# Performance work log

Hardware: AMD Instinct MI355X
Metric: run time of the kernel (lower is better)

Reference implementation:

```python
import jax, jax.numpy as jnp
import numpy as np
from jax.scipy.linalg import block_diag

N_STATE, N_INPUT, HORIZON = 32, 16, 64


def setup_inputs() -> dict:
    key = jax.random.key(0)
    kA, kB, kC, kx = jax.random.split(key, 4)
    n_all = N_STATE + N_INPUT
    A = jax.random.normal(kA, (N_STATE, N_STATE), dtype=jnp.float32)
    B = jax.random.normal(kB, (N_STATE, N_INPUT), dtype=jnp.float32)
    Craw = jax.random.normal(kC, (HORIZON, n_all, n_all), dtype=jnp.float32)
    # symmetric positive-definite stage costs -> nonsingular KKT system
    C = jnp.einsum('tij,tkj->tik', Craw, Craw) / jnp.sqrt(jnp.float32(n_all)) \
        + jnp.eye(n_all, dtype=jnp.float32)
    x0 = jax.random.normal(kx, (N_STATE,), dtype=jnp.float32)
    return {"A": A, "B": B, "C": C, "T": HORIZON, "x0": x0}


def reference(A, B, C, T, x0):
    n_state = A.shape[0]
    n_input = B.shape[1]
    n_all = n_state + n_input
    dt = A.dtype

    # cost_mat: block-diagonal [n_all*T, n_all*T]
    cost_mat = block_diag(*C)

    # dynamics: [n_state*T, n_all*T]
    AB = jnp.concatenate((A, B), axis=1)              # [n_state, n_all]
    AB_blk = block_diag(*([AB] * (T - 1)))            # [(T-1)*n_state, (T-1)*n_all]
    dynamics = jnp.zeros((n_state * T, n_all * T), dtype=dt)
    dynamics = dynamics.at[:n_state, :n_state].set(jnp.eye(n_state, dtype=dt))
    dynamics = dynamics.at[n_state:n_state + (T - 1) * n_state,
                           :(T - 1) * n_all].set(AB_blk)
    # -I coupling entries: row n_state*t + i, col n_all*t + i, t=1..T-1
    t = jnp.arange(1, T)
    rows = (n_state * t)[:, None] + jnp.arange(n_state)[None, :]
    cols = (n_all * t)[:, None] + jnp.arange(n_state)[None, :]
    dynamics = dynamics.at[rows, cols].set(jnp.asarray(-1.0, dt))

    zero_mat = jnp.zeros((n_state * T, n_state * T), dtype=dt)
    full_mat = jnp.block([[cost_mat, dynamics.T],
                          [dynamics, zero_mat]])      # [(n_all+n_state)*T]^2

    # rhs: zeros except x0 at the start of the dynamics block
    sol = jnp.zeros(n_all * T + n_state * T, dtype=dt)
    sol = sol.at[n_all * T: n_all * T + n_state].set(x0)

    tau_mu = jnp.linalg.solve(full_mat, sol[:, None])[:, 0]
    tau_star = tau_mu[:n_all * T]
    mu_star = tau_mu[n_all * T:]
    return tau_star, mu_star
```

## Files before the change

kernel.cpp:

```cpp
#include <hip/hip_runtime.h>


namespace {

constexpr int NS  = 32;
constexpr int NI  = 16;
constexpr int NA  = 48;
constexpr int TT  = 64;
constexpr int NTH = 256;
constexpr int NBLK = 64;

using ull = unsigned long long;

__device__ __forceinline__ void fma4(float4& a, float s, const float4& b) {
  a.x += s * b.x; a.y += s * b.y; a.z += s * b.z; a.w += s * b.w;
}
__device__ __forceinline__ void fms4(float4& a, float s, const float4& b) {
  a.x -= s * b.x; a.y -= s * b.y; a.z -= s * b.z; a.w -= s * b.w;
}
__device__ __forceinline__ float dot4(const float4& a, const float4& b) {
  return a.x * b.x + a.y * b.y + a.z * b.z + a.w * b.w;
}
__device__ __forceinline__ float rdlane(float v, int l) {
  return __int_as_float(__builtin_amdgcn_readlane(__float_as_int(v), l));
}

__device__ __forceinline__ ull ald(const ull* p) {
  return __hip_atomic_load(p, __ATOMIC_RELAXED, __HIP_MEMORY_SCOPE_AGENT);
}
__device__ __forceinline__ void ast(ull* p, ull v) {
  __hip_atomic_store(p, v, __ATOMIC_RELAXED, __HIP_MEMORY_SCOPE_AGENT);
}
__device__ __forceinline__ ull pack2(float x, float y) {
  return (ull)__float_as_uint(x) | ((ull)__float_as_uint(y) << 32);
}
__device__ __forceinline__ float2 unpack2(ull v) {
  return make_float2(__uint_as_float((unsigned)v),
                     __uint_as_float((unsigned)(v >> 32)));
}
__device__ __forceinline__ float4 ald4(const ull* p) {
  ull lo = ald(p), hi = ald(p + 1);
  float2 a = unpack2(lo), b = unpack2(hi);
  return make_float4(a.x, a.y, b.x, b.y);
}
__device__ __forceinline__ void ast4(ull* p, const float4& v) {
  ast(p, pack2(v.x, v.y)); ast(p + 1, pack2(v.z, v.w));
}

__device__ __forceinline__ unsigned fld(const unsigned* f) {
  return __hip_atomic_load(f, __ATOMIC_RELAXED, __HIP_MEMORY_SCOPE_AGENT);
}
__device__ __forceinline__ void fst(unsigned* f) {
  __hip_atomic_store(f, 1u, __ATOMIC_RELAXED, __HIP_MEMORY_SCOPE_AGENT);
}
__device__ __forceinline__ void waitf(const unsigned* f) {
  if (threadIdx.x == 0)
    while (fld(f) == 0) __builtin_amdgcn_s_sleep(1);
  __syncthreads();
}
__device__ __forceinline__ void setf(unsigned* f) {
  asm volatile("s_waitcnt vmcnt(0)" ::: "memory");
  __syncthreads();
  if (threadIdx.x == 0) fst(f);
}

template<int K>
__device__ __forceinline__ void tile_outer(const float* Acol0, int lda,
                                           const float* Bcol0, int ldb,
                                           float4 acc[4]) {
  #pragma unroll
  for (int m = 0; m < K; ++m) {
    const float4 va = *(const float4*)(Acol0 + m * lda);
    const float4 vb = *(const float4*)(Bcol0 + m * ldb);
    fma4(acc[0], va.x, vb); fma4(acc[1], va.y, vb);
    fma4(acc[2], va.z, vb); fma4(acc[3], va.w, vb);
  }
}

template<int KQ>
__device__ __forceinline__ void tile_dot(const float* Arow0, int lda,
                                         const float* Brow0, int ldb,
                                         float acc[4][4]) {
  #pragma unroll
  for (int q = 0; q < KQ; ++q) {
    float4 va[4], vb[4];
    #pragma unroll
    for (int r = 0; r < 4; ++r) va[r] = *(const float4*)(Arow0 + r * lda + 4 * q);
    #pragma unroll
    for (int c = 0; c < 4; ++c) vb[c] = *(const float4*)(Brow0 + c * ldb + 4 * q);
    #pragma unroll
    for (int r = 0; r < 4; ++r)
      #pragma unroll
      for (int c = 0; c < 4; ++c) acc[r][c] += dot4(va[r], vb[c]);
  }
}

__device__ __forceinline__ float step_dot(const float4 m[8], float x) {
  float a0 = 0.f, a1 = 0.f, a2 = 0.f, a3 = 0.f;
  #pragma unroll
  for (int q = 0; q < 8; ++q) {
    a0 += rdlane(x, 4 * q + 0) * m[q].x;
    a1 += rdlane(x, 4 * q + 1) * m[q].y;
    a2 += rdlane(x, 4 * q + 2) * m[q].z;
    a3 += rdlane(x, 4 * q + 3) * m[q].w;
  }
  return (a0 + a1) + (a2 + a3);
}

__device__ __forceinline__ int nlev(int rm) {
  return (rm == TT - 1) ? 0 : (32 - __clz(TT - 1 - rm));
}

__global__ __launch_bounds__(NTH, 1) void lqr_all(
    const float* __restrict__ A, const float* __restrict__ Bm,
    const float* __restrict__ C, const float* __restrict__ x0,
    float* __restrict__ out,
    float* __restrict__ Sb0, float* __restrict__ Sb1,
    float* __restrict__ Mall, unsigned* __restrict__ flg) {
  __shared__ float sC [NA][NA];
  __shared__ float sAB[NS][NA];
  __shared__ float sRiST[NS][NI];
  __shared__ float sBRi [NS][NI];
  __shared__ float sAi[NS][NS], sCi[NS][NS], sJi[NS][NS];
  __shared__ float sAj[NS][NS], sCj[NS][NS], sJj[NS][NS];
  __shared__ float sAjT[NS][36];
  __shared__ float sV[NS][NS], sU[NS][NS];
  __shared__ float sY1[NS][NS], sY2[NS][NS], sW[NS][NS];
  __shared__ float sX[NS][NS], sZm[NS][NS];
  __shared__ float sG[NS][NA], sFu[NI][NA], sK[NI][NS], sK2[NI][NS];
  __shared__ float sXt0[NS], sXt1[NS];

  const int t = ((blockIdx.x & 7) << 3) | (blockIdx.x >> 3);
  const int tid = threadIdx.x, lane = tid & 63, wid = tid >> 6;
  unsigned* wr = flg;
  unsigned* rd = flg + 448;
  unsigned* mf = flg + 832;

  {
    const float* Ct = C + (size_t)t * NA * NA;
    for (int e = tid; e < NA * NA; e += NTH) sC[e / NA][e % NA] = Ct[e];
    for (int e = tid; e < NS * NA; e += NTH) {
      int i = e / NA, j = e % NA;
      sAB[i][j] = (j < NS) ? A[i * NS + j] : Bm[i * NI + (j - NS)];
    }
    __syncthreads();
    if (wid < 2 && lane < 48) {
      const int c = lane;
      float f[NI];
      if (c < NI) {
        #pragma unroll
        for (int i = 0; i < NI; ++i) f[i] = sC[NS + i][NS + c];
      } else {
        const int a = c - NI;
        if (wid == 0) {
          #pragma unroll
          for (int i = 0; i < NI; ++i) f[i] = sC[a][NS + i];
        } else {
          #pragma unroll
          for (int i = 0; i < NI; ++i) f[i] = sAB[a][NS + i];
        }
      }
      #pragma unroll
      for (int k = 0; k < NI; ++k) {
        float mi[NI];
        #pragma unroll
        for (int i = 0; i < NI; ++i) mi[i] = rdlane(f[i], k);
        const float inv = 1.0f / mi[k];
        f[k] *= inv;
        #pragma unroll
        for (int i = 0; i < NI; ++i) if (i != k) f[i] -= mi[i] * f[k];
      }
      if (c >= NI) {
        const int a = c - NI;
        float* D = (wid == 0) ? &sRiST[a][0] : &sBRi[a][0];
        #pragma unroll
        for (int i = 0; i < NI; ++i) D[i] = f[i];
      }
    }
    __syncthreads();
    ull* outA = (ull*)(Sb0 + (size_t)t * 3072);
    ull* outC = outA + 512;
    ull* outJ = outA + 1024;
    if (tid < 64) {
      const int a = tid >> 3, b = tid & 7;
      float acc[4][4];
      #pragma unroll
      for (int r = 0; r < 4; ++r)
        #pragma unroll
        for (int c = 0; c < 4; ++c) acc[r][c] = 0.f;
      tile_dot<4>(&sRiST[4 * a][0], NI, &sC[4 * b][NS], NA, acc);
      #pragma unroll
      for (int r = 0; r < 4; ++r) {
        const float4 q4 = *(const float4*)&sC[4 * a + r][4 * b];
        const float4 v = make_float4(q4.x - acc[r][0], q4.y - acc[r][1],
                                     q4.z - acc[r][2], q4.w - acc[r][3]);
        *(float4*)&sJi[4 * a + r][4 * b] = v;
        ast4(outJ + ((4 * a + r) * NS + 4 * b) / 2, v);
      }
    } else if (tid < 128) {
      const int q = tid - 64, a = q >> 3, b = q & 7;
      float acc[4][4];
      #pragma unroll
      for (int r = 0; r < 4; ++r)
        #pragma unroll
        for (int c = 0; c < 4; ++c) acc[r][c] = 0.f;
      tile_dot<4>(&sBRi[4 * a][0], NI, &sC[4 * b][NS], NA, acc);
      #pragma unroll
      for (int r = 0; r < 4; ++r) {
        const float4 a4 = *(const float4*)&sAB[4 * a + r][4 * b];
        const float4 v = make_float4(a4.x - acc[r][0], a4.y - acc[r][1],
                                     a4.z - acc[r][2], a4.w - acc[r][3]);
        *(float4*)&sAi[4 * a + r][4 * b] = v;
        ast4(outA + ((4 * a + r) * NS + 4 * b) / 2, v);
      }
    } else if (tid < 192) {
      const int q = tid - 128, a = q >> 3, b = q & 7;
      float acc[4][4];
      #pragma unroll
      for (int r = 0; r < 4; ++r)
        #pragma unroll
        for (int c = 0; c < 4; ++c) acc[r][c] = 0.f;
      tile_dot<4>(&sBRi[4 * a][0], NI, &sAB[4 * b][NS], NA, acc);
      #pragma unroll
      for (int r = 0; r < 4; ++r) {
        const float4 v = make_float4(acc[r][0], acc[r][1], acc[r][2], acc[r][3]);
        *(float4*)&sCi[4 * a + r][4 * b] = v;
        ast4(outC + ((4 * a + r) * NS + 4 * b) / 2, v);
      }
    }
  }
  setf(&wr[0 * 64 + t]);

  auto combine = [&]() {
    #pragma unroll
    for (int r = 0; r < 4; ++r) {
      const int e = tid + 256 * r, i = e >> 5, j = e & 31;
      sAjT[j][i] = sAj[i][j];
    }
    if (tid < 64) {
      const int a = tid >> 3, b = tid & 7;
      float4 acc[4] = {make_float4(0,0,0,0), make_float4(0,0,0,0),
                       make_float4(0,0,0,0), make_float4(0,0,0,0)};
      tile_outer<NS>(&sCi[0][4 * a], NS, &sJj[0][4 * b], NS, acc);
      if (a == b) { acc[0].x += 1.f; acc[1].y += 1.f; acc[2].z += 1.f; acc[3].w += 1.f; }
      #pragma unroll
      for (int r = 0; r < 4; ++r) *(float4*)&sX[4 * a + r][4 * b] = acc[r];
    }
    __syncthreads();
    if (wid < 2) {
      const int c = lane;
      float f[NS];
      if (c < NS) {
        #pragma unroll
        for (int i = 0; i < NS; ++i) f[i] = sX[i][c];
      } else if (wid == 0) {
        #pragma unroll
        for (int i = 0; i < NS; ++i) f[i] = sAi[i][c - NS];
      } else {
        #pragma unroll
        for (int i = 0; i < NS; ++i) f[i] = sCi[i][c - NS];
      }
      #pragma unroll
      for (int k = 0; k < NS; ++k) {
        float mi[NS];
        #pragma unroll
        for (int i = 0; i < NS; ++i) mi[i] = rdlane(f[i], k);
        const float inv = 1.0f / mi[k];
        f[k] *= inv;
        #pragma unroll
        for (int i = 0; i < NS; ++i) if (i != k) f[i] -= mi[i] * f[k];
      }
      if (c >= NS) {
        const int col = c - NS;
        if (wid == 0) {
          #pragma unroll
          for (int i = 0; i < NS; ++i) sV[i][col] = f[i];
        } else {
          #pragma unroll
          for (int i = 0; i < NS; ++i) sU[i][col] = f[i];
        }
      }
    }
    __syncthreads();
    if (tid < 192) {
      const int grp = tid >> 6, q = tid & 63, a = q >> 3, b = q & 7;
      float4 acc[4] = {make_float4(0,0,0,0), make_float4(0,0,0,0),
                       make_float4(0,0,0,0), make_float4(0,0,0,0)};
      if (grp == 0) {
        tile_outer<NS>(&sJj[0][4 * a], NS, &sV[0][4 * b], NS, acc);
        #pragma unroll
        for (int r = 0; r < 4; ++r) *(float4*)&sW[4 * a + r][4 * b] = acc[r];
      } else if (grp == 1) {
        tile_outer<NS>(&sAjT[0][4 * a], 36, &sV[0][4 * b], NS, acc);
        #pragma unroll
        for (int r = 0; r < 4; ++r) *(float4*)&sX[4 * a + r][4 * b] = acc[r];
      } else {
        tile_outer<NS>(&sAjT[0][4 * a], 36, &sU[0][4 * b], NS, acc);
        #pragma unroll
        for (int r = 0; r < 4; ++r) *(float4*)&sZm[4 * a + r][4 * b] = acc[r];
      }
    }
    __syncthreads();
    if (tid < 64) {
      const int a = tid >> 3, b = tid & 7;
      float4 acc[4] = {make_float4(0,0,0,0), make_float4(0,0,0,0),
                       make_float4(0,0,0,0), make_float4(0,0,0,0)};
      tile_outer<NS>(&sAi[0][4 * a], NS, &sW[0][4 * b], NS, acc);
      #pragma unroll
      for (int r = 0; r < 4; ++r) {
        const float4 j4 = *(const float4*)&sJi[4 * a + r][4 * b];
        acc[r].x += j4.x; acc[r].y += j4.y; acc[r].z += j4.z; acc[r].w += j4.w;
        *(float4*)&sY1[4 * a + r][4 * b] = acc[r];
      }
    } else if (tid < 128) {
      const int q = tid - 64, a = q >> 3, b = q & 7;
      float acc[4][4];
      #pragma unroll
      for (int r = 0; r < 4; ++r)
        #pragma unroll
        for (int c = 0; c < 4; ++c) acc[r][c] = 0.f;
      tile_dot<8>(&sZm[4 * a][0], NS, &sAj[4 * b][0], NS, acc);
      #pragma unroll
      for (int r = 0; r < 4; ++r) {
        const float4 c4 = *(const float4*)&sCj[4 * a + r][4 * b];
        *(float4*)&sY2[4 * a + r][4 * b] =
            make_float4(acc[r][0] + c4.x, acc[r][1] + c4.y,
                        acc[r][2] + c4.z, acc[r][3] + c4.w);
      }
    }
    __syncthreads();
    ((ull*)sAi)[tid] = ((const ull*)sX)[tid];
    ((ull*)sAi)[tid + 256] = ((const ull*)sX)[tid + 256];
    ((ull*)sCi)[tid] = ((const ull*)sY2)[tid];
    ((ull*)sCi)[tid + 256] = ((const ull*)sY2)[tid + 256];
    ((ull*)sJi)[tid] = ((const ull*)sY1)[tid];
    ((ull*)sJi)[tid + 256] = ((const ull*)sY1)[tid + 256];
    __syncthreads();
  };

  for (int l = 0; l < 6; ++l) {
    const int off = 1 << l;
    const int rm = t + off;
    if (rm < TT) {
      const int nlv = nlev(rm);
      const int v = (l < nlv) ? l : nlv;
      const float* Sin = (v & 1) ? Sb1 : Sb0;
      float* Sout = ((l + 1) & 1) ? Sb1 : Sb0;
      ull* Eo = (ull*)(Sout + (size_t)t * 3072);
      waitf(&wr[v * 64 + rm]);
      const ull* Ej = (const ull*)(Sin + (size_t)rm * 3072);
      {
        ull r0 = ald(Ej + tid),        r1 = ald(Ej + 256 + tid);
        ull r2 = ald(Ej + 512 + tid),  r3 = ald(Ej + 768 + tid);
        ull r4 = ald(Ej + 1024 + tid), r5 = ald(Ej + 1280 + tid);
        ((ull*)sAj)[tid] = r0; ((ull*)sAj)[tid + 256] = r1;
        ((ull*)sCj)[tid] = r2; ((ull*)sCj)[tid + 256] = r3;
        ((ull*)sJj)[tid] = r4; ((ull*)sJj)[tid + 256] = r5;
      }
      __syncthreads();
      if (v == l && tid == 0) fst(&rd[l * 64 + rm]);
      combine();
      if (l >= 1 && t >= (off >> 1)) waitf(&rd[(l - 1) * 64 + t]);
      ast(Eo + tid,        ((const ull*)sAi)[tid]);
      ast(Eo + 256 + tid,  ((const ull*)sAi)[tid + 256]);
      ast(Eo + 512 + tid,  ((const ull*)sCi)[tid]);
      ast(Eo + 768 + tid,  ((const ull*)sCi)[tid + 256]);
      ast(Eo + 1024 + tid, ((const ull*)sJi)[tid]);
      ast(Eo + 1280 + tid, ((const ull*)sJi)[tid + 256]);
      setf(&wr[(l + 1) * 64 + t]);
    }
  }

  auto kmat = [&](int tau, bool hasP, float (*Pm)[NS], float (*Kd)[NS], bool wM) {
    const int ui = tid / 12, uk = tid - 12 * ui;
    float4 cr0 = make_float4(0,0,0,0), cr1 = make_float4(0,0,0,0);
    float4 cr2 = make_float4(0,0,0,0), cr3 = make_float4(0,0,0,0);
    if (tid < 48) {
      const float* Ct = C + (size_t)tau * NA * NA;
      cr0 = *(const float4*)&Ct[(NS + 4 * ui + 0) * NA + 4 * uk];
      cr1 = *(const float4*)&Ct[(NS + 4 * ui + 1) * NA + 4 * uk];
      cr2 = *(const float4*)&Ct[(NS + 4 * ui + 2) * NA + 4 * uk];
      cr3 = *(const float4*)&Ct[(NS + 4 * ui + 3) * NA + 4 * uk];
    }
    if (hasP) {
      if (tid < 96) {
        const int gi = tid / 12, gk = tid - 12 * gi;
        float4 acc[4] = {make_float4(0,0,0,0), make_float4(0,0,0,0),
                         make_float4(0,0,0,0), make_float4(0,0,0,0)};
        tile_outer<NS>(&Pm[0][4 * gi], NS, &sAB[0][4 * gk], NA, acc);
        #pragma unroll
        for (int r = 0; r < 4; ++r) *(float4*)&sG[4 * gi + r][4 * gk] = acc[r];
      }
    } else {
      for (int e = tid; e < NS * NA; e += NTH) sG[e / NA][e % NA] = 0.f;
    }
    __syncthreads();
    if (tid < 48) {
      float4 acc[4] = {cr0, cr1, cr2, cr3};
      tile_outer<NS>(&sAB[0][NS + 4 * ui], NA, &sG[0][4 * uk], NA, acc);
      #pragma unroll
      for (int r = 0; r < 4; ++r) *(float4*)&sFu[4 * ui + r][4 * uk] = acc[r];
    }
    __syncthreads();
    if (wid == 0) {
      const int col = (lane < 16) ? (NS + lane) : (lane - 16);
      float f[NI];
      #pragma unroll
      for (int i = 0; i < NI; ++i) f[i] = sFu[i][col];
      #pragma unroll
      for (int k = 0; k < NI; ++k) {
        float mi[NI];
        #pragma unroll
        for (int i = 0; i < NI; ++i) mi[i] = rdlane(f[i], k);
        const float inv = 1.0f / mi[k];
        f[k] *= inv;
        #pragma unroll
        for (int i = 0; i < NI; ++i) if (i != k) f[i] -= mi[i] * f[k];
      }
      if (lane >= 16 && lane < 48) {
        const int b = lane - 16;
        #pragma unroll
        for (int i = 0; i < NI; ++i) Kd[i][b] = f[i];
      }
    }
    __syncthreads();
    if (wM && tid < 64) {
      const int ma = tid >> 3, mb = tid & 7;
      float4 a0 = *(const float4*)&sAB[4 * ma + 0][4 * mb];
      float4 a1 = *(const float4*)&sAB[4 * ma + 1][4 * mb];
      float4 a2 = *(const float4*)&sAB[4 * ma + 2][4 * mb];
      float4 a3 = *(const float4*)&sAB[4 * ma + 3][4 * mb];
      #pragma unroll
      for (int q = 0; q < 4; ++q) {
        const float4 vf0 = *(const float4*)&sAB[4 * ma + 0][NS + 4 * q];
        const float4 vf1 = *(const float4*)&sAB[4 * ma + 1][NS + 4 * q];
        const float4 vf2 = *(const float4*)&sAB[4 * ma + 2][NS + 4 * q];
        const float4 vf3 = *(const float4*)&sAB[4 * ma + 3][NS + 4 * q];
        #pragma unroll
        for (int d = 0; d < 4; ++d) {
          const float4 vkk = *(const float4*)&Kd[4 * q + d][4 * mb];
          const float s0 = (d == 0) ? vf0.x : (d == 1) ? vf0.y : (d == 2) ? vf0.z : vf0.w;
          const float s1 = (d == 0) ? vf1.x : (d == 1) ? vf1.y : (d == 2) ? vf1.z : vf1.w;
          const float s2 = (d == 0) ? vf2.x : (d == 1) ? vf2.y : (d == 2) ? vf2.z : vf2.w;
          const float s3 = (d == 0) ? vf3.x : (d == 1) ? vf3.y : (d == 2) ? vf3.z : vf3.w;
          fms4(a0, s0, vkk); fms4(a1, s1, vkk); fms4(a2, s2, vkk); fms4(a3, s3, vkk);
        }
      }
      ull* Mt = (ull*)(Mall + (size_t)tau * NS * NS);
      ast4(Mt + (4 * ma + 0) * 16 + 2 * mb, a0);
      ast4(Mt + (4 * ma + 1) * 16 + 2 * mb, a1);
      ast4(Mt + (4 * ma + 2) * 16 + 2 * mb, a2);
      ast4(Mt + (4 * ma + 3) * 16 + 2 * mb, a3);
    }
    __syncthreads();
  };

  if (t >= 1) kmat(t - 1, true, sJi, sK, true);
  if (t == TT - 1) kmat(TT - 1, false, nullptr, sK2, false);
  setf(&mf[t]);

  {
    if (tid < NBLK) {
      while (fld(&mf[tid]) == 0) __builtin_amdgcn_s_sleep(1);
    }
    __syncthreads();
    if (wid == 0) {
      const int i = lane;
      if (i < NS) {
        const ull* Mg = (const ull*)Mall;
        float4 mA[8], mB[8];
        float x = x0[i];
        if (t == 1) sXt1[i] = x;
        if (t >= 1) {
          #pragma unroll
          for (int q = 0; q < 8; ++q) mA[q] = ald4(Mg + 0 * 512 + i * 16 + 2 * q);
        }
        if (t >= 2) {
          #pragma unroll
          for (int q = 0; q < 8; ++q) mB[q] = ald4(Mg + 1 * 512 + i * 16 + 2 * q);
        }
        for (int s = 0; s < t; s += 2) {
          x = step_dot(mA, x);
          if (s + 1 == t - 1) sXt1[i] = x;
          if (s + 2 < t) {
            #pragma unroll
            for (int q = 0; q < 8; ++q)
              mA[q] = ald4(Mg + (s + 2) * 512 + i * 16 + 2 * q);
          }
          if (s + 1 < t) {
            x = step_dot(mB, x);
            if (s + 2 == t - 1) sXt1[i] = x;
            if (s + 3 < t) {
              #pragma unroll
              for (int q = 0; q < 8; ++q)
                mB[q] = ald4(Mg + (s + 3) * 512 + i * 16 + 2 * q);
            }
          }
        }
        sXt0[i] = x;
        out[t * NA + i] = x;
      }
    }
    __syncthreads();
  }

  {
    if (t >= 1 && tid < NI) {
      const float4* Kr = (const float4*)&sK[tid][0];
      const float4* xr = (const float4*)sXt1;
      float acc = 0.f;
      #pragma unroll
      for (int q = 0; q < 8; ++q) acc += dot4(Kr[q], xr[q]);
      out[(t - 1) * NA + NS + tid] = -acc;
    } else if (tid >= NI && tid < NI + NS) {
      const int i = tid - NI;
      const float4* Pr = (const float4*)&sJi[i][0];
      const float4* xr = (const float4*)sXt0;
      float acc = 0.f;
      #pragma unroll
      for (int q = 0; q < 8; ++q) acc += dot4(Pr[q], xr[q]);
      out[NA * TT + t * NS + i] = (t == 0) ? -acc : acc;
    } else if (t == TT - 1 && tid >= 192 && tid < 192 + NI) {
      const int i = tid - 192;
      const float4* Kr = (const float4*)&sK2[i][0];
      const float4* xr = (const float4*)sXt0;
      float acc = 0.f;
      #pragma unroll
      for (int q = 0; q < 8; ++q) acc += dot4(Kr[q], xr[q]);
      out[(TT - 1) * NA + NS + i] = -acc;
    }
  }
}

}

extern "C" void kernel_launch(void* const* d_in, const int* in_sizes, int n_in,
                              void* d_out, int out_size, void* d_ws, size_t ws_size,
                              hipStream_t stream) {
  const float* A  = (const float*)d_in[0];
  const float* Bm = (const float*)d_in[1];
  const float* C  = (const float*)d_in[2];
  const float* x0 = (const float*)d_in[4];
  float* out = (float*)d_out;

  float* Sb0 = (float*)d_ws;
  float* Sb1 = Sb0 + (size_t)TT * 3072;
  float* Mall = Sb1 + (size_t)TT * 3072;
  unsigned* flg = (unsigned*)(Mall + (size_t)TT * NS * NS);

  hipMemsetAsync(flg, 0, 4096, stream);
  hipLaunchKernelGGL(lqr_all, dim3(NBLK), dim3(NTH), 0, stream,
                     A, Bm, C, x0, out, Sb0, Sb1, Mall, flg);
}
```

Baseline: 126.6 us.

## Switch parallel scan to radix-4 levels with dual concurrent combines

Replaces the six-level radix-2 associative scan over time steps with a three-level radix-4 scan. Each block now waits for and loads up to three neighbour elements per level. Two of the combines run concurrently on half-block partitions, followed by a full-block combine. This cuts the number of cross-block synchronisation rounds and global flag waits, in exchange for more work per level, counted read-done flags, and heavier shared-memory use. Shared buffers are aliased to fit the extra staging.

New measurement: 139.6 us. 1.1x slower.

```diff
diff --git a/kernel.cpp b/kernel.cpp
--- a/kernel.cpp
+++ b/kernel.cpp
@@ -107,8 +107,8 @@
   return (a0 + a1) + (a2 + a3);
 }
 
-__device__ __forceinline__ int nlev(int rm) {
-  return (rm == TT - 1) ? 0 : (32 - __clz(TT - 1 - rm));
+__device__ __forceinline__ int nlev4(int rm) {
+  return (rm < 48) ? 3 : (rm < 60) ? 2 : (rm < 63) ? 1 : 0;
 }
 
 __global__ __launch_bounds__(NTH, 1) void lqr_all(
@@ -117,24 +117,25 @@
     float* __restrict__ out,
     float* __restrict__ Sb0, float* __restrict__ Sb1,
     float* __restrict__ Mall, unsigned* __restrict__ flg) {
-  __shared__ float sC [NA][NA];
+  __shared__ float sScr[NA * NA];
   __shared__ float sAB[NS][NA];
   __shared__ float sRiST[NS][NI];
   __shared__ float sBRi [NS][NI];
   __shared__ float sAi[NS][NS], sCi[NS][NS], sJi[NS][NS];
-  __shared__ float sAj[NS][NS], sCj[NS][NS], sJj[NS][NS];
-  __shared__ float sAjT[NS][36];
-  __shared__ float sV[NS][NS], sU[NS][NS];
-  __shared__ float sY1[NS][NS], sY2[NS][NS], sW[NS][NS];
-  __shared__ float sX[NS][NS], sZm[NS][NS];
-  __shared__ float sG[NS][NA], sFu[NI][NA], sK[NI][NS], sK2[NI][NS];
+  __shared__ float sE[3][3][NS][NS];
+  __shared__ float sAjT[2][NS][36];
+  __shared__ float sXs[2][NS][NS], sVs[2][NS][NS], sUs[2][NS][NS];
+  __shared__ float sWs[2][NS][NS], sZs[2][NS][NS];
+  __shared__ float sK[NI][NS], sK2[NI][NS];
   __shared__ float sXt0[NS], sXt1[NS];
 
   const int t = ((blockIdx.x & 7) << 3) | (blockIdx.x >> 3);
   const int tid = threadIdx.x, lane = tid & 63, wid = tid >> 6;
-  unsigned* wr = flg;
-  unsigned* rd = flg + 448;
-  unsigned* mf = flg + 832;
+  unsigned* wr  = flg;
+  unsigned* rdc = flg + 256;
+  unsigned* mf  = flg + 448;
+
+  float (*sC)[NA] = (float(*)[NA])sScr;
 
   {
     const float* Ct = C + (size_t)t * NA * NA;
@@ -231,20 +232,23 @@
   }
   setf(&wr[0 * 64 + t]);
 
-  auto combine = [&]() {
+  auto combine_full = [&](float (*RA)[NS], float (*RC)[NS], float (*RJ)[NS]) {
+    float (*T)[36] = sAjT[0];
+    float (*X)[NS] = sXs[0]; float (*V)[NS] = sVs[0]; float (*U)[NS] = sUs[0];
+    float (*W)[NS] = sWs[0]; float (*Z)[NS] = sZs[0];
     #pragma unroll
     for (int r = 0; r < 4; ++r) {
       const int e = tid + 256 * r, i = e >> 5, j = e & 31;
-      sAjT[j][i] = sAj[i][j];
+      T[j][i] = RA[i][j];
     }
     if (tid < 64) {
       const int a = tid >> 3, b = tid & 7;
       float4 acc[4] = {make_float4(0,0,0,0), make_float4(0,0,0,0),
                        make_float4(0,0,0,0), make_float4(0,0,0,0)};
-      tile_outer<NS>(&sCi[0][4 * a], NS, &sJj[0][4 * b], NS, acc);
+      tile_outer<NS>(&sCi[0][4 * a], NS, &RJ[0][4 * b], NS, acc);
       if (a == b) { acc[0].x += 1.f; acc[1].y += 1.f; acc[2].z += 1.f; acc[3].w += 1.f; }
       #pragma unroll
-      for (int r = 0; r < 4; ++r) *(float4*)&sX[4 * a + r][4 * b] = acc[r];
+      for (int r = 0; r < 4; ++r) *(float4*)&X[4 * a + r][4 * b] = acc[r];
     }
     __syncthreads();
     if (wid < 2) {
@@ -252,7 +256,7 @@
       float f[NS];
       if (c < NS) {
         #pragma unroll
-        for (int i = 0; i < NS; ++i) f[i] = sX[i][c];
+        for (int i = 0; i < NS; ++i) f[i] = X[i][c];
       } else if (wid == 0) {
         #pragma unroll
         for (int i = 0; i < NS; ++i) f[i] = sAi[i][c - NS];
@@ -272,13 +276,9 @@
       }
       if (c >= NS) {
         const int col = c - NS;
-        if (wid == 0) {
-          #pragma unroll
-          for (int i = 0; i < NS; ++i) sV[i][col] = f[i];
-        } else {
-          #pragma unroll
-          for (int i = 0; i < NS; ++i) sU[i][col] = f[i];
-        }
+        float (*D)[NS] = (wid == 0) ? V : U;
+        #pragma unroll
+        for (int i = 0; i < NS; ++i) D[i][col] = f[i];
       }
     }
     __syncthreads();
@@ -287,17 +287,17 @@
       float4 acc[4] = {make_float4(0,0,0,0), make_float4(0,0,0,0),
                        make_float4(0,0,0,0), make_float4(0,0,0,0)};
       if (grp == 0) {
-        tile_outer<NS>(&sJj[0][4 * a], NS, &sV[0][4 * b], NS, acc);
-        #pragma unroll
-        for (int r = 0; r < 4; ++r) *(float4*)&sW[4 * a + r][4 * b] = acc[r];
+        tile_outer<NS>(&RJ[0][4 * a], NS, &V[0][4 * b], NS, acc);
+        #pragma unroll
+        for (int r = 0; r < 4; ++r) *(float4*)&W[4 * a + r][4 * b] = acc[r];
       } else if (grp == 1) {
-        tile_outer<NS>(&sAjT[0][4 * a], 36, &sV[0][4 * b], NS, acc);
-        #pragma unroll
-        for (int r = 0; r < 4; ++r) *(float4*)&sX[4 * a + r][4 * b] = acc[r];
+        tile_outer<NS>(&T[0][4 * a], 36, &V[0][4 * b], NS, acc);
+        #pragma unroll
+        for (int r = 0; r < 4; ++r) *(float4*)&X[4 * a + r][4 * b] = acc[r];
       } else {
-        tile_outer<NS>(&sAjT[0][4 * a], 36, &sU[0][4 * b], NS, acc);
-        #pragma unroll
-        for (int r = 0; r < 4; ++r) *(float4*)&sZm[4 * a + r][4 * b] = acc[r];
+        tile_outer<NS>(&T[0][4 * a], 36, &U[0][4 * b], NS, acc);
+        #pragma unroll
+        for (int r = 0; r < 4; ++r) *(float4*)&Z[4 * a + r][4 * b] = acc[r];
       }
     }
     __syncthreads();
@@ -305,12 +305,12 @@
       const int a = tid >> 3, b = tid & 7;
       float4 acc[4] = {make_float4(0,0,0,0), make_float4(0,0,0,0),
                        make_float4(0,0,0,0), make_float4(0,0,0,0)};
-      tile_outer<NS>(&sAi[0][4 * a], NS, &sW[0][4 * b], NS, acc);
+      tile_outer<NS>(&sAi[0][4 * a], NS, &W[0][4 * b], NS, acc);
       #pragma unroll
       for (int r = 0; r < 4; ++r) {
         const float4 j4 = *(const float4*)&sJi[4 * a + r][4 * b];
         acc[r].x += j4.x; acc[r].y += j4.y; acc[r].z += j4.z; acc[r].w += j4.w;
-        *(float4*)&sY1[4 * a + r][4 * b] = acc[r];
+        *(float4*)&sJi[4 * a + r][4 * b] = acc[r];
       }
     } else if (tid < 128) {
       const int q = tid - 64, a = q >> 3, b = q & 7;
@@ -319,58 +319,194 @@
       for (int r = 0; r < 4; ++r)
         #pragma unroll
         for (int c = 0; c < 4; ++c) acc[r][c] = 0.f;
-      tile_dot<8>(&sZm[4 * a][0], NS, &sAj[4 * b][0], NS, acc);
+      tile_dot<8>(&Z[4 * a][0], NS, &RA[4 * b][0], NS, acc);
       #pragma unroll
       for (int r = 0; r < 4; ++r) {
-        const float4 c4 = *(const float4*)&sCj[4 * a + r][4 * b];
-        *(float4*)&sY2[4 * a + r][4 * b] =
+        const float4 c4 = *(const float4*)&RC[4 * a + r][4 * b];
+        *(float4*)&sCi[4 * a + r][4 * b] =
             make_float4(acc[r][0] + c4.x, acc[r][1] + c4.y,
                         acc[r][2] + c4.z, acc[r][3] + c4.w);
       }
     }
     __syncthreads();
-    ((ull*)sAi)[tid] = ((const ull*)sX)[tid];
-    ((ull*)sAi)[tid + 256] = ((const ull*)sX)[tid + 256];
-    ((ull*)sCi)[tid] = ((const ull*)sY2)[tid];
-    ((ull*)sCi)[tid + 256] = ((const ull*)sY2)[tid + 256];
-    ((ull*)sJi)[tid] = ((const ull*)sY1)[tid];
-    ((ull*)sJi)[tid + 256] = ((const ull*)sY1)[tid + 256];
+    ((ull*)sAi)[tid] = ((const ull*)X)[tid];
+    ((ull*)sAi)[tid + 256] = ((const ull*)X)[tid + 256];
     __syncthreads();
   };
 
-  for (int l = 0; l < 6; ++l) {
-    const int off = 1 << l;
-    const int rm = t + off;
-    if (rm < TT) {
-      const int nlv = nlev(rm);
-      const int v = (l < nlv) ? l : nlv;
-      const float* Sin = (v & 1) ? Sb1 : Sb0;
-      float* Sout = ((l + 1) & 1) ? Sb1 : Sb0;
-      ull* Eo = (ull*)(Sout + (size_t)t * 3072);
-      waitf(&wr[v * 64 + rm]);
-      const ull* Ej = (const ull*)(Sin + (size_t)rm * 3072);
-      {
-        ull r0 = ald(Ej + tid),        r1 = ald(Ej + 256 + tid);
-        ull r2 = ald(Ej + 512 + tid),  r3 = ald(Ej + 768 + tid);
-        ull r4 = ald(Ej + 1024 + tid), r5 = ald(Ej + 1280 + tid);
-        ((ull*)sAj)[tid] = r0; ((ull*)sAj)[tid + 256] = r1;
-        ((ull*)sCj)[tid] = r2; ((ull*)sCj)[tid + 256] = r3;
-        ((ull*)sJj)[tid] = r4; ((ull*)sJj)[tid + 256] = r5;
-      }
+  auto combine_dual = [&]() {
+    const int p = tid >> 7, tp = tid & 127, pw = (tid >> 6) & 1, pl = tid & 63;
+    float (*LA)[NS] = p ? sE[1][0] : sAi;
+    float (*LC)[NS] = p ? sE[1][1] : sCi;
+    float (*LJ)[NS] = p ? sE[1][2] : sJi;
+    float (*RA)[NS] = p ? sE[2][0] : sE[0][0];
+    float (*RC)[NS] = p ? sE[2][1] : sE[0][1];
+    float (*RJ)[NS] = p ? sE[2][2] : sE[0][2];
+    float (*T)[36] = sAjT[p];
+    float (*X)[NS] = sXs[p]; float (*V)[NS] = sVs[p]; float (*U)[NS] = sUs[p];
+    float (*W)[NS] = sWs[p]; float (*Z)[NS] = sZs[p];
+    #pragma unroll
+    for (int r = 0; r < 8; ++r) {
+      const int e = tp + 128 * r, i = e >> 5, j = e & 31;
+      T[j][i] = RA[i][j];
+    }
+    if (tp < 64) {
+      const int a = tp >> 3, b = tp & 7;
+      float4 acc[4] = {make_float4(0,0,0,0), make_float4(0,0,0,0),
+                       make_float4(0,0,0,0), make_float4(0,0,0,0)};
+      tile_outer<NS>(&LC[0][4 * a], NS, &RJ[0][4 * b], NS, acc);
+      if (a == b) { acc[0].x += 1.f; acc[1].y += 1.f; acc[2].z += 1.f; acc[3].w += 1.f; }
+      #pragma unroll
+      for (int r = 0; r < 4; ++r) *(float4*)&X[4 * a + r][4 * b] = acc[r];
+    }
+    __syncthreads();
+    {
+      const int c = pl;
+      float f[NS];
+      if (c < NS) {
+        #pragma unroll
+        for (int i = 0; i < NS; ++i) f[i] = X[i][c];
+      } else if (pw == 0) {
+        #pragma unroll
+        for (int i = 0; i < NS; ++i) f[i] = LA[i][c - NS];
+      } else {
+        #pragma unroll
+        for (int i = 0; i < NS; ++i) f[i] = LC[i][c - NS];
+      }
+      #pragma unroll
+      for (int k = 0; k < NS; ++k) {
+        float mi[NS];
+        #pragma unroll
+        for (int i = 0; i < NS; ++i) mi[i] = rdlane(f[i], k);
+        const float inv = 1.0f / mi[k];
+        f[k] *= inv;
+        #pragma unroll
+        for (int i = 0; i < NS; ++i) if (i != k) f[i] -= mi[i] * f[k];
+      }
+      if (c >= NS) {
+        const int col = c - NS;
+        float (*D)[NS] = (pw == 0) ? V : U;
+        #pragma unroll
+        for (int i = 0; i < NS; ++i) D[i][col] = f[i];
+      }
+    }
+    __syncthreads();
+    for (int u = tp; u < 192; u += 128) {
+      const int grp = u >> 6, q = u & 63, a = q >> 3, b = q & 7;
+      float4 acc[4] = {make_float4(0,0,0,0), make_float4(0,0,0,0),
+                       make_float4(0,0,0,0), make_float4(0,0,0,0)};
+      if (grp == 0) {
+        tile_outer<NS>(&RJ[0][4 * a], NS, &V[0][4 * b], NS, acc);
+        #pragma unroll
+        for (int r = 0; r < 4; ++r) *(float4*)&W[4 * a + r][4 * b] = acc[r];
+      } else if (grp == 1) {
+        tile_outer<NS>(&T[0][4 * a], 36, &V[0][4 * b], NS, acc);
+        #pragma unroll
+        for (int r = 0; r < 4; ++r) *(float4*)&X[4 * a + r][4 * b] = acc[r];
+      } else {
+        tile_outer<NS>(&T[0][4 * a], 36, &U[0][4 * b], NS, acc);
+        #pragma unroll
+        for (int r = 0; r < 4; ++r) *(float4*)&Z[4 * a + r][4 * b] = acc[r];
+      }
+    }
+    __syncthreads();
+    {
+      const int grp = tp >> 6, q = tp & 63, a = q >> 3, b = q & 7;
+      if (grp == 0) {
+        float4 acc[4] = {make_float4(0,0,0,0), make_float4(0,0,0,0),
+                         make_float4(0,0,0,0), make_float4(0,0,0,0)};
+        tile_outer<NS>(&LA[0][4 * a], NS, &W[0][4 * b], NS, acc);
+        #pragma unroll
+        for (int r = 0; r < 4; ++r) {
+          const float4 j4 = *(const float4*)&LJ[4 * a + r][4 * b];
+          acc[r].x += j4.x; acc[r].y += j4.y; acc[r].z += j4.z; acc[r].w += j4.w;
+          *(float4*)&LJ[4 * a + r][4 * b] = acc[r];
+        }
+      } else {
+        float acc[4][4];
+        #pragma unroll
+        for (int r = 0; r < 4; ++r)
+          #pragma unroll
+          for (int c = 0; c < 4; ++c) acc[r][c] = 0.f;
+        tile_dot<8>(&Z[4 * a][0], NS, &RA[4 * b][0], NS, acc);
+        #pragma unroll
+        for (int r = 0; r < 4; ++r) {
+          const float4 c4 = *(const float4*)&RC[4 * a + r][4 * b];
+          *(float4*)&LC[4 * a + r][4 * b] =
+              make_float4(acc[r][0] + c4.x, acc[r][1] + c4.y,
+                          acc[r][2] + c4.z, acc[r][3] + c4.w);
+        }
+      }
+    }
+    __syncthreads();
+    #pragma unroll
+    for (int r = 0; r < 4; ++r)
+      ((ull*)LA)[tp + 128 * r] = ((const ull*)X)[tp + 128 * r];
+    __syncthreads();
+  };
+
+  for (int l = 0; l < 3; ++l) {
+    const int off = 1 << (2 * l);
+    if (t + off >= TT) break;
+    int nr = 0; int rms[3]; int vs[3];
+    #pragma unroll
+    for (int k = 1; k <= 3; ++k) {
+      const int rm = t + k * off;
+      if (rm < TT) {
+        rms[nr] = rm;
+        const int nl = nlev4(rm);
+        vs[nr] = (l < nl) ? l : nl;
+        ++nr;
+      }
+    }
+    if (tid == 0) {
+      for (int q = 0; q < nr; ++q)
+        while (fld(&wr[vs[q] * 64 + rms[q]]) == 0) __builtin_amdgcn_s_sleep(1);
+    }
+    __syncthreads();
+    for (int q = 0; q < nr; ++q) {
+      const float* Sin = (vs[q] & 1) ? Sb1 : Sb0;
+      const ull* Ej = (const ull*)(Sin + (size_t)rms[q] * 3072);
+      ull r0 = ald(Ej + tid),        r1 = ald(Ej + 256 + tid);
+      ull r2 = ald(Ej + 512 + tid),  r3 = ald(Ej + 768 + tid);
+      ull r4 = ald(Ej + 1024 + tid), r5 = ald(Ej + 1280 + tid);
+      ((ull*)sE[q][0])[tid] = r0; ((ull*)sE[q][0])[tid + 256] = r1;
+      ((ull*)sE[q][1])[tid] = r2; ((ull*)sE[q][1])[tid + 256] = r3;
+      ((ull*)sE[q][2])[tid] = r4; ((ull*)sE[q][2])[tid + 256] = r5;
+    }
+    __syncthreads();
+    if (tid == 0) {
+      for (int q = 0; q < nr; ++q)
+        if (vs[q] == l) atomicAdd(&rdc[l * 64 + rms[q]], 1u);
+    }
+    if (nr == 3) {
+      combine_dual();
+      combine_full(sE[1][0], sE[1][1], sE[1][2]);
+    } else if (nr == 2) {
+      combine_full(sE[0][0], sE[0][1], sE[0][2]);
+      combine_full(sE[1][0], sE[1][1], sE[1][2]);
+    } else {
+      combine_full(sE[0][0], sE[0][1], sE[0][2]);
+    }
+    if (l >= 1) {
+      const unsigned need = (3u < (unsigned)(t >> (2 * (l - 1))))
+                                ? 3u : (unsigned)(t >> (2 * (l - 1)));
+      if (tid == 0)
+        while (fld(&rdc[(l - 1) * 64 + t]) < need) __builtin_amdgcn_s_sleep(1);
       __syncthreads();
-      if (v == l && tid == 0) fst(&rd[l * 64 + rm]);
-      combine();
-      if (l >= 1 && t >= (off >> 1)) waitf(&rd[(l - 1) * 64 + t]);
-      ast(Eo + tid,        ((const ull*)sAi)[tid]);
-      ast(Eo + 256 + tid,  ((const ull*)sAi)[tid + 256]);
-      ast(Eo + 512 + tid,  ((const ull*)sCi)[tid]);
-      ast(Eo + 768 + tid,  ((const ull*)sCi)[tid + 256]);
-      ast(Eo + 1024 + tid, ((const ull*)sJi)[tid]);
-      ast(Eo + 1280 + tid, ((const ull*)sJi)[tid + 256]);
-      setf(&wr[(l + 1) * 64 + t]);
-    }
+    }
+    ull* Eo = (ull*)((((l + 1) & 1) ? Sb1 : Sb0) + (size_t)t * 3072);
+    ast(Eo + tid,        ((const ull*)sAi)[tid]);
+    ast(Eo + 256 + tid,  ((const ull*)sAi)[tid + 256]);
+    ast(Eo + 512 + tid,  ((const ull*)sCi)[tid]);
+    ast(Eo + 768 + tid,  ((const ull*)sCi)[tid + 256]);
+    ast(Eo + 1024 + tid, ((const ull*)sJi)[tid]);
+    ast(Eo + 1280 + tid, ((const ull*)sJi)[tid + 256]);
+    setf(&wr[(l + 1) * 64 + t]);
   }
 
+  float (*sG)[NA]  = (float(*)[NA])sScr;
+  float (*sFu)[NA] = (float(*)[NA])(sScr + NS * NA);
   auto kmat = [&](int tau, bool hasP, float (*Pm)[NS], float (*Kd)[NS], bool wM) {
     const int ui = tid / 12, uk = tid - 12 * ui;
     float4 cr0 = make_float4(0,0,0,0), cr1 = make_float4(0,0,0,0);
```
